# Kernel tuning notes

Hardware: AMD Instinct MI355X
Metric: run time of the kernel (lower is better)

## Reference

```python
import jax, jax.numpy as jnp
import numpy as np

NEG_INF = -jnp.inf


def setup_inputs() -> dict:
    B, T, E, H = 16, 1024, 1024, 1024  # batch, seq, embed_dim, head_dim (T <= H required by original buffer slicing)
    key = jax.random.key(0)
    k1, k2, k3, k4, k5, k6 = jax.random.split(key, 6)
    return {
        "key": jax.random.normal(k1, (B, T, E), dtype=jnp.float32),
        "query": jax.random.normal(k2, (B, T, E), dtype=jnp.float32),
        "value": jax.random.normal(k3, (B, T, E), dtype=jnp.float32),
        "padding_mask": jnp.zeros((B, 1, T), dtype=jnp.int32),
        # nn.Linear(embed_dim, head_dim, bias=False) weights: [head_dim, embed_dim]
        "Wk": jax.random.normal(k4, (H, E), dtype=jnp.float32) * (E ** -0.5),
        "Wq": jax.random.normal(k5, (H, E), dtype=jnp.float32) * (E ** -0.5),
        "Wv": jax.random.normal(k6, (H, E), dtype=jnp.float32) * (E ** -0.5),
    }


def reference(key, query, value, padding_mask, Wk, Wq, Wv):
    # key/query/value: [B, T, E]; W*: [H, E]
    B, T, E = key.shape
    k = jnp.einsum("bte,he->bth", key, Wk)
    q = jnp.einsum("bte,he->bth", query, Wq)
    v = jnp.einsum("bte,he->bth", value, Wv)
    # NOTE: original scales by d_k = key.size(-1) = embed_dim, not head_dim
    scale = 1.0 / jnp.sqrt(jnp.float32(E))
    qk = jnp.einsum("bth,bsh->bts", q, k) * scale  # [B, T, T]
    # causal buffer is tril(ones, diagonal=1): position i can attend to j <= i+1
    causal = jnp.tril(jnp.ones((T, T), dtype=jnp.float32), k=1)
    qk = jnp.where(causal == 0, NEG_INF, qk)
    qk = jnp.where(padding_mask == 1, NEG_INF, qk)  # padding_mask broadcasts [B,1,T] -> [B,T,T]
    p = jax.nn.softmax(qk, axis=-1)
    attn = jnp.einsum("bts,bsh->bth", p, v)  # dropout is identity in eval mode
    return attn
```

## Files before the change

### kernel.cpp

```cpp
#include <hip/hip_runtime.h>
#include <hip/hip_bf16.h>
#include <stdint.h>

typedef __bf16 bf16;
typedef __attribute__((ext_vector_type(8))) __bf16 bf16x8;
typedef __attribute__((ext_vector_type(4))) __bf16 bf16x4;
typedef __attribute__((ext_vector_type(4))) float  f32x4;

static __device__ __forceinline__ void gll16(const void* g, void* lds_base) {
  __builtin_amdgcn_global_load_lds((__attribute__((address_space(1))) void*)g,
                                   (__attribute__((address_space(3))) void*)lds_base,
                                   16, 0, 0);
}

#define MFMA_CLUSTER(MQ)                                                       \
  __builtin_amdgcn_s_barrier();                                                \
  asm volatile("s_waitcnt lgkmcnt(0)" ::: "memory");                           \
  __builtin_amdgcn_sched_barrier(0);                                           \
  __builtin_amdgcn_s_setprio(1);                                               \
  _Pragma("unroll") for (int i_ = 0; i_ < 4; ++i_)                             \
  _Pragma("unroll") for (int n_ = 0; n_ < 4; ++n_)                             \
  _Pragma("unroll") for (int kh_ = 0; kh_ < 2; ++kh_)                          \
    acc[(MQ) * 4 + i_][n_] = __builtin_amdgcn_mfma_f32_16x16x32_bf16(          \
        af[i_][kh_], bfr[n_][kh_], acc[(MQ) * 4 + i_][n_], 0, 0, 0);           \
  __builtin_amdgcn_s_setprio(0);

template <int VARIANT>
__global__ __launch_bounds__(512, 2) void gemm8(const bf16* __restrict__ A,
                                                const bf16* __restrict__ B,
                                                bf16* __restrict__ Cb,
                                                float* __restrict__ Cf,
                                                const int* __restrict__ pad) {
  extern __shared__ char smem[];
  char* ldsA = smem;
  char* ldsB = smem + 65536;

  const int tid = threadIdx.x;
  const int lane = tid & 63, wave = tid >> 6;
  const int lo = lane & 15, hi = lane >> 4;
  const int wmi = wave >> 2, wni = wave & 3;
  const int swz = (lo & 7) << 4;

  const int nwg = gridDim.x;
  const int id = (blockIdx.x % 8) * (nwg >> 3) + blockIdx.x / 8;

  int row0, col0, nt, b = 0;
  if (VARIANT <= 1) {
    row0 = (id >> 2) * 256; col0 = (id & 3) * 256; nt = 16;
  } else {
    b = id >> 4;
    const int r = id & 15, it = r >> 2, jt = r & 3;
    row0 = it * 256; col0 = jt * 256;
    nt = (VARIANT == 3) ? min(16, 4 * it + 6) : 16;
    if (VARIANT == 2 && jt > it + 1) return;
    if (VARIANT == 2 && jt == it + 1) {
      bf16* Sb = Cb + ((size_t)b << 20);
      bf16x8 z = {};
#pragma unroll
      for (int q = 0; q < 16; ++q) {
        const int off = (q * 512 + tid) * 8;
        *(bf16x8*)(Sb + (size_t)(row0 + (off >> 8)) * 1024 + col0 + (off & 255)) = z;
      }
      return;
    }
  }
  const bf16* Ap = A + ((size_t)b << 20) + (size_t)row0 * 1024;
  const bf16* Bp = B + ((size_t)b << 20) + (size_t)col0 * 1024;
  const int ntm1 = nt - 1;

  auto stgA = [&](int tidx, int slot) {
    const int tc = tidx > ntm1 ? ntm1 : tidx;
#pragma unroll
    for (int r = 0; r < 4; ++r) {
      const int x  = (wave * 4 + r) * 1024 + lane * 16;
      const int xs = x ^ (((x >> 7) & 7) << 4);
      gll16((const char*)Ap + (size_t)(xs >> 7) * 2048 + (size_t)tc * 128 + (xs & 127),
            ldsA + slot * 32768 + (wave * 4 + r) * 1024);
    }
  };
  auto stgB = [&](int tidx, int slot) {
    const int tc = tidx > ntm1 ? ntm1 : tidx;
#pragma unroll
    for (int r = 0; r < 4; ++r) {
      const int x  = (wave * 4 + r) * 1024 + lane * 16;
      const int xs = x ^ (((x >> 7) & 7) << 4);
      gll16((const char*)Bp + (size_t)(xs >> 7) * 2048 + (size_t)tc * 128 + (xs & 127),
            ldsB + slot * 32768 + (wave * 4 + r) * 1024);
    }
  };

  f32x4 acc[8][4] = {};

  stgB(0, 0);
  stgA(0, 0);
  stgB(1, 1);
  asm volatile("s_waitcnt vmcnt(4)" ::: "memory");
  __builtin_amdgcn_s_barrier();

  bf16x8 af[4][2], bfr[4][2];
#pragma unroll 2
  for (int u = 0; u < nt; ++u) {
    const int cur = u & 1;
#pragma unroll
    for (int i_ = 0; i_ < 4; ++i_)
#pragma unroll
      for (int kh_ = 0; kh_ < 2; ++kh_) {
        const int row_ = wmi * 128 + i_ * 16 + lo;
        af[i_][kh_] = *(const bf16x8*)(ldsA + cur * 32768 +
                                       ((row_ * 128 + kh_ * 64 + hi * 16) ^ swz));
      }
#pragma unroll
    for (int n_ = 0; n_ < 4; ++n_)
#pragma unroll
      for (int kh_ = 0; kh_ < 2; ++kh_) {
        const int row_ = wni * 64 + n_ * 16 + lo;
        bfr[n_][kh_] = *(const bf16x8*)(ldsB + cur * 32768 +
                                        ((row_ * 128 + kh_ * 64 + hi * 16) ^ swz));
      }
    stgA(u + 1, cur ^ 1);
    MFMA_CLUSTER(0)
    __builtin_amdgcn_s_barrier();
#pragma unroll
    for (int i_ = 0; i_ < 4; ++i_)
#pragma unroll
      for (int kh_ = 0; kh_ < 2; ++kh_) {
        const int row_ = wmi * 128 + 64 + i_ * 16 + lo;
        af[i_][kh_] = *(const bf16x8*)(ldsA + cur * 32768 +
                                       ((row_ * 128 + kh_ * 64 + hi * 16) ^ swz));
      }
    stgB(u + 2, cur);
    MFMA_CLUSTER(1)
    asm volatile("s_waitcnt vmcnt(4)" ::: "memory");
    __builtin_amdgcn_s_barrier();
  }

  if (VARIANT == 0) {
#pragma unroll
    for (int m = 0; m < 8; ++m)
#pragma unroll
      for (int n = 0; n < 4; ++n) {
        const int c = col0 + wni * 64 + n * 16 + lo;
        const int rbase = row0 + wmi * 128 + m * 16 + hi * 4;
#pragma unroll
        for (int j = 0; j < 4; ++j)
          Cb[(size_t)(rbase + j) * 1024 + c] = (bf16)acc[m][n][j];
      }
  } else if (VARIANT == 1) {
#pragma unroll
    for (int m = 0; m < 8; ++m)
#pragma unroll
      for (int n = 0; n < 4; ++n) {
        const int r = row0 + wmi * 128 + m * 16 + hi * 4;
        const int c = col0 + wni * 64 + n * 16 + lo;
        const int bb = r >> 10, tt = r & 1023;
        bf16x4 h = { (bf16)acc[m][n][0], (bf16)acc[m][n][1],
                     (bf16)acc[m][n][2], (bf16)acc[m][n][3] };
        *(bf16x4*)(Cb + ((size_t)bb << 20) + ((size_t)c << 10) + tt) = h;
      }
  } else if (VARIANT == 2) {
    const float NINF = -__builtin_inff();
#pragma unroll
    for (int n = 0; n < 4; ++n) {
      const int s = col0 + wni * 64 + n * 16 + lo;
      const int pd = pad[(b << 10) + s];
#pragma unroll
      for (int m = 0; m < 8; ++m) {
        const int tbase = row0 + wmi * 128 + m * 16 + hi * 4;
#pragma unroll
        for (int j = 0; j < 4; ++j) {
          float v = acc[m][n][j] * 0.03125f;
          if (s > tbase + j + 1) v = 0.f;
          else if (pd != 0) v = NINF;
          Cb[((size_t)b << 20) + (size_t)(tbase + j) * 1024 + s] = (bf16)v;
        }
      }
    }
  } else {
#pragma unroll
    for (int m = 0; m < 8; ++m)
#pragma unroll
      for (int n = 0; n < 4; ++n) {
        const int h2 = col0 + wni * 64 + n * 16 + lo;
        const int tbase = row0 + wmi * 128 + m * 16 + hi * 4;
#pragma unroll
        for (int j = 0; j < 4; ++j)
          Cf[((size_t)b << 20) + (size_t)(tbase + j) * 1024 + h2] = acc[m][n][j];
      }
  }
  asm volatile("s_waitcnt vmcnt(0)" ::: "memory");
}

__global__ __launch_bounds__(256) void cvt_kernel(const float* __restrict__ src,
                                                  bf16* __restrict__ dst, int n) {
  const int i = (blockIdx.x * 256 + threadIdx.x) * 8;
  if (i >= n) return;
  const f32x4 a = *(const f32x4*)(src + i);
  const f32x4 b = *(const f32x4*)(src + i + 4);
  bf16x8 o = { (bf16)a[0], (bf16)a[1], (bf16)a[2], (bf16)a[3],
               (bf16)b[0], (bf16)b[1], (bf16)b[2], (bf16)b[3] };
  *(bf16x8*)(dst + i) = o;
}

__global__ __launch_bounds__(256) void cvtW_kernel(const float* __restrict__ s0,
                                                   const float* __restrict__ s1,
                                                   const float* __restrict__ s2,
                                                   bf16* __restrict__ d0,
                                                   bf16* __restrict__ d1,
                                                   bf16* __restrict__ d2) {
  const int seg = blockIdx.x >> 9, blk = blockIdx.x & 511;
  const float* src = seg == 0 ? s0 : (seg == 1 ? s1 : s2);
  bf16* dst = seg == 0 ? d0 : (seg == 1 ? d1 : d2);
  const int i = (blk * 256 + threadIdx.x) * 8;
  const f32x4 a = *(const f32x4*)(src + i);
  const f32x4 b = *(const f32x4*)(src + i + 4);
  bf16x8 o = { (bf16)a[0], (bf16)a[1], (bf16)a[2], (bf16)a[3],
               (bf16)b[0], (bf16)b[1], (bf16)b[2], (bf16)b[3] };
  *(bf16x8*)(dst + i) = o;
}

__global__ __launch_bounds__(64) void corner_kernel(const bf16* __restrict__ Q,
                                                    const bf16* __restrict__ K,
                                                    const int* __restrict__ pad,
                                                    bf16* __restrict__ S) {
  const int b = blockIdx.x / 3, it = blockIdx.x % 3;
  const int t = it * 256 + 255, s = (it + 1) * 256;
  const int lane = threadIdx.x;
  const bf16* q = Q + ((size_t)b << 20) + (size_t)t * 1024 + lane * 16;
  const bf16* k = K + ((size_t)b << 20) + (size_t)s * 1024 + lane * 16;
  bf16x8 q0 = *(const bf16x8*)q, q1 = *(const bf16x8*)(q + 8);
  bf16x8 k0 = *(const bf16x8*)k, k1 = *(const bf16x8*)(k + 8);
  float d = 0.f;
#pragma unroll
  for (int j = 0; j < 8; ++j) d += (float)q0[j] * (float)k0[j] + (float)q1[j] * (float)k1[j];
#pragma unroll
  for (int o = 32; o; o >>= 1) d += __shfl_xor(d, o, 64);
  if (lane == 0) {
    float v = d * 0.03125f;
    if (pad[(b << 10) + s] != 0) v = -__builtin_inff();
    S[((size_t)b << 20) + (size_t)t * 1024 + s] = (bf16)v;
  }
}

__global__ __launch_bounds__(256) void softmax_kernel(bf16* __restrict__ S) {
  const int row  = blockIdx.x * 4 + (threadIdx.x >> 6);
  const int lane = threadIdx.x & 63;
  const int t = row & 1023;
  const int w = min(1024, t + 2);
  const bool act = lane * 16 < w;
  bf16* r = S + (size_t)row * 1024 + lane * 16;
  bf16x8 v0 = {}, v1 = {};
  float f[16];
#pragma unroll
  for (int j = 0; j < 16; ++j) f[j] = -1e30f;
  if (act) {
    v0 = *(const bf16x8*)r;
    v1 = *(const bf16x8*)(r + 8);
#pragma unroll
    for (int j = 0; j < 16; ++j)
      if (lane * 16 + j < w) f[j] = (float)(j < 8 ? v0[j] : v1[j - 8]);
  }
  float m = f[0];
#pragma unroll
  for (int j = 1; j < 16; ++j) m = fmaxf(m, f[j]);
#pragma unroll
  for (int o = 32; o; o >>= 1) m = fmaxf(m, __shfl_xor(m, o, 64));
  float sum = 0.f;
  float e[16];
#pragma unroll
  for (int j = 0; j < 16; ++j) { e[j] = __expf(f[j] - m); sum += e[j]; }
#pragma unroll
  for (int o = 32; o; o >>= 1) sum += __shfl_xor(sum, o, 64);
  const float inv = 1.0f / sum;
  if (act) {
#pragma unroll
    for (int j = 0; j < 8; ++j) {
      v0[j] = (bf16)(lane * 16 + j < w ? e[j] * inv : 0.f);
      v1[j] = (bf16)(lane * 16 + 8 + j < w ? e[8 + j] * inv : 0.f);
    }
    *(bf16x8*)r = v0;
    *(bf16x8*)(r + 8) = v1;
  }
}

extern "C" void kernel_launch(void* const* d_in, const int* in_sizes, int n_in,
                              void* d_out, int out_size, void* d_ws, size_t ws_size,
                              hipStream_t stream) {
  const float* key   = (const float*)d_in[0];
  const float* query = (const float*)d_in[1];
  const float* value = (const float*)d_in[2];
  const int*   pad   = (const int*)d_in[3];
  const float* Wk    = (const float*)d_in[4];
  const float* Wq    = (const float*)d_in[5];
  const float* Wv    = (const float*)d_in[6];
  float* out = (float*)d_out;

  bf16* Wkb = (bf16*)d_ws;
  bf16* Wqb = Wkb + (1 << 20);
  bf16* Wvb = Wqb + (1 << 20);
  bf16* qb  = Wvb + (1 << 20);
  bf16* kb  = qb  + (16 << 20);
  bf16* vT  = kb  + (16 << 20);
  bf16* S   = vT  + (16 << 20);
  bf16* Xb  = S;

  hipFuncSetAttribute(reinterpret_cast<const void*>(&gemm8<0>),
                      hipFuncAttributeMaxDynamicSharedMemorySize, 131072);
  hipFuncSetAttribute(reinterpret_cast<const void*>(&gemm8<1>),
                      hipFuncAttributeMaxDynamicSharedMemorySize, 131072);
  hipFuncSetAttribute(reinterpret_cast<const void*>(&gemm8<2>),
                      hipFuncAttributeMaxDynamicSharedMemorySize, 131072);
  hipFuncSetAttribute(reinterpret_cast<const void*>(&gemm8<3>),
                      hipFuncAttributeMaxDynamicSharedMemorySize, 131072);

  cvtW_kernel<<<1536, 256, 0, stream>>>(Wk, Wq, Wv, Wkb, Wqb, Wvb);

  cvt_kernel<<<8192, 256, 0, stream>>>(query, Xb, 16 << 20);
  gemm8<0><<<256, 512, 131072, stream>>>(Xb, Wqb, qb, nullptr, nullptr);
  cvt_kernel<<<8192, 256, 0, stream>>>(key, Xb, 16 << 20);
  gemm8<0><<<256, 512, 131072, stream>>>(Xb, Wkb, kb, nullptr, nullptr);
  cvt_kernel<<<8192, 256, 0, stream>>>(value, Xb, 16 << 20);
  gemm8<1><<<256, 512, 131072, stream>>>(Xb, Wvb, vT, nullptr, nullptr);

  gemm8<2><<<256, 512, 131072, stream>>>(qb, kb, S, nullptr, pad);
  corner_kernel<<<48, 64, 0, stream>>>(qb, kb, pad, S);
  softmax_kernel<<<4096, 256, 0, stream>>>(S);
  gemm8<3><<<256, 512, 131072, stream>>>(S, vT, nullptr, out, nullptr);
}
```

Baseline: 248.5 us.

## Fuse fp32-to-bf16 input conversion into projection GEMM A-operand staging

Removes the three standalone conversion kernels for query, key and value. The projection GEMM variants now load fp32 activations into registers, convert them to bf16 and write them into swizzled LDS, with a reworked software pipeline that splits A staging into two halves interleaved with MFMA clusters. This is meant to remove the write and re-read of the bf16 intermediate and the extra kernel launches. In exchange, the A operand loses asynchronous global-to-LDS loads, register pressure rises, and there are extra full vmcnt waits that may expose latency.

```diff
diff --git a/kernel.cpp b/kernel.cpp
--- a/kernel.cpp
+++ b/kernel.cpp
@@ -12,6 +12,11 @@
                                    (__attribute__((address_space(3))) void*)lds_base,
                                    16, 0, 0);
 }
+
+#define BARR  __builtin_amdgcn_s_barrier()
+#define VMW(N) asm volatile("s_waitcnt vmcnt(" #N ")" ::: "memory")
+#define LGKM0 asm volatile("s_waitcnt lgkmcnt(0)" ::: "memory")
+#define SB0   __builtin_amdgcn_sched_barrier(0)
 
 #define MFMA_CLUSTER(MQ)                                                       \
   __builtin_amdgcn_s_barrier();                                                \
@@ -22,15 +27,16 @@
   _Pragma("unroll") for (int n_ = 0; n_ < 4; ++n_)                             \
   _Pragma("unroll") for (int kh_ = 0; kh_ < 2; ++kh_)                          \
     acc[(MQ) * 4 + i_][n_] = __builtin_amdgcn_mfma_f32_16x16x32_bf16(          \
-        af[i_][kh_], bfr[n_][kh_], acc[(MQ) * 4 + i_][n_], 0, 0, 0);           \
+        af2[i_][kh_], bfr[n_][kh_], acc[(MQ) * 4 + i_][n_], 0, 0, 0);          \
   __builtin_amdgcn_s_setprio(0);
 
 template <int VARIANT>
-__global__ __launch_bounds__(512, 2) void gemm8(const bf16* __restrict__ A,
+__global__ __launch_bounds__(512, 2) void gemm8(const void* __restrict__ Araw,
                                                 const bf16* __restrict__ B,
                                                 bf16* __restrict__ Cb,
                                                 float* __restrict__ Cf,
                                                 const int* __restrict__ pad) {
+  constexpr bool FP32A = (VARIANT <= 1);
   extern __shared__ char smem[];
   char* ldsA = smem;
   char* ldsB = smem + 65536;
@@ -64,20 +70,12 @@
       return;
     }
   }
-  const bf16* Ap = A + ((size_t)b << 20) + (size_t)row0 * 1024;
-  const bf16* Bp = B + ((size_t)b << 20) + (size_t)col0 * 1024;
   const int ntm1 = nt - 1;
-
-  auto stgA = [&](int tidx, int slot) {
-    const int tc = tidx > ntm1 ? ntm1 : tidx;
-#pragma unroll
-    for (int r = 0; r < 4; ++r) {
-      const int x  = (wave * 4 + r) * 1024 + lane * 16;
-      const int xs = x ^ (((x >> 7) & 7) << 4);
-      gll16((const char*)Ap + (size_t)(xs >> 7) * 2048 + (size_t)tc * 128 + (xs & 127),
-            ldsA + slot * 32768 + (wave * 4 + r) * 1024);
-    }
-  };
+  const float* Afp = FP32A ? (const float*)Araw + (size_t)row0 * 1024 : nullptr;
+  const bf16*  Ab  = FP32A ? nullptr
+                           : (const bf16*)Araw + ((size_t)b << 20) + (size_t)row0 * 1024;
+  const bf16*  Bp  = B + (FP32A ? (size_t)0 : ((size_t)b << 20)) + (size_t)col0 * 1024;
+
   auto stgB = [&](int tidx, int slot) {
     const int tc = tidx > ntm1 ? ntm1 : tidx;
 #pragma unroll
@@ -88,50 +86,143 @@
             ldsB + slot * 32768 + (wave * 4 + r) * 1024);
     }
   };
+  auto stgA = [&](int tidx, int slot) {
+    const int tc = tidx > ntm1 ? ntm1 : tidx;
+#pragma unroll
+    for (int r = 0; r < 4; ++r) {
+      const int x  = (wave * 4 + r) * 1024 + lane * 16;
+      const int xs = x ^ (((x >> 7) & 7) << 4);
+      gll16((const char*)Ab + (size_t)(xs >> 7) * 2048 + (size_t)tc * 128 + (xs & 127),
+            ldsA + slot * 32768 + (wave * 4 + r) * 1024);
+    }
+  };
 
   f32x4 acc[8][4] = {};
-
-  stgB(0, 0);
-  stgA(0, 0);
-  stgB(1, 1);
-  asm volatile("s_waitcnt vmcnt(4)" ::: "memory");
-  __builtin_amdgcn_s_barrier();
-
-  bf16x8 af[4][2], bfr[4][2];
+  bf16x8 bfr[4][2];
+
+  auto rdBall = [&](int slot) {
+#pragma unroll
+    for (int n = 0; n < 4; ++n)
+#pragma unroll
+      for (int kh = 0; kh < 2; ++kh) {
+        const int row = wni * 64 + n * 16 + lo;
+        bfr[n][kh] = *(const bf16x8*)(ldsB + slot * 32768 +
+                                      ((row * 128 + kh * 64 + hi * 16) ^ swz));
+      }
+  };
+
+  if constexpr (FP32A) {
+    bf16x8 af[4];
+    f32x4 rQ[4];
+    auto glbAh = [&](int h, int t) {
+      const int tc = t > ntm1 ? ntm1 : t;
+      const float* p = Afp + (size_t)(h * 128 + (tid >> 2)) * 1024 +
+                       (size_t)tc * 64 + (tid & 3) * 16;
+      rQ[0] = *(const f32x4*)(p);
+      rQ[1] = *(const f32x4*)(p + 4);
+      rQ[2] = *(const f32x4*)(p + 8);
+      rQ[3] = *(const f32x4*)(p + 12);
+    };
+    auto wrAh = [&](int h, int slot) {
+      const int row = h * 128 + (tid >> 2);
+      const int base = row * 128 + (tid & 3) * 32;
+      const int key = (row & 7) << 4;
+      char* d = ldsA + slot * 32768;
+      bf16x8 o0 = { (bf16)rQ[0][0], (bf16)rQ[0][1], (bf16)rQ[0][2], (bf16)rQ[0][3],
+                    (bf16)rQ[1][0], (bf16)rQ[1][1], (bf16)rQ[1][2], (bf16)rQ[1][3] };
+      bf16x8 o1 = { (bf16)rQ[2][0], (bf16)rQ[2][1], (bf16)rQ[2][2], (bf16)rQ[2][3],
+                    (bf16)rQ[3][0], (bf16)rQ[3][1], (bf16)rQ[3][2], (bf16)rQ[3][3] };
+      *(bf16x8*)(d + (base ^ key)) = o0;
+      *(bf16x8*)(d + ((base + 16) ^ key)) = o1;
+    };
+    auto rdAk = [&](int mh, int kh, int slot) {
+#pragma unroll
+      for (int i = 0; i < 4; ++i) {
+        const int row = wmi * 128 + mh * 64 + i * 16 + lo;
+        af[i] = *(const bf16x8*)(ldsA + slot * 32768 +
+                                 ((row * 128 + kh * 64 + hi * 16) ^ swz));
+      }
+    };
+    auto mmaK = [&](int mh, int kh) {
+#pragma unroll
+      for (int i = 0; i < 4; ++i)
+#pragma unroll
+        for (int n = 0; n < 4; ++n)
+          acc[mh * 4 + i][n] = __builtin_amdgcn_mfma_f32_16x16x32_bf16(
+              af[i], bfr[n][kh], acc[mh * 4 + i][n], 0, 0, 0);
+    };
+
+    glbAh(0, 0); VMW(0); wrAh(0, 0);
+    glbAh(1, 0); VMW(0); wrAh(1, 0);
+    stgB(0, 0); stgB(1, 1);
+    VMW(4);
+    LGKM0; BARR;
+
 #pragma unroll 2
-  for (int u = 0; u < nt; ++u) {
-    const int cur = u & 1;
-#pragma unroll
-    for (int i_ = 0; i_ < 4; ++i_)
-#pragma unroll
-      for (int kh_ = 0; kh_ < 2; ++kh_) {
-        const int row_ = wmi * 128 + i_ * 16 + lo;
-        af[i_][kh_] = *(const bf16x8*)(ldsA + cur * 32768 +
-                                       ((row_ * 128 + kh_ * 64 + hi * 16) ^ swz));
-      }
-#pragma unroll
-    for (int n_ = 0; n_ < 4; ++n_)
-#pragma unroll
-      for (int kh_ = 0; kh_ < 2; ++kh_) {
-        const int row_ = wni * 64 + n_ * 16 + lo;
-        bfr[n_][kh_] = *(const bf16x8*)(ldsB + cur * 32768 +
-                                        ((row_ * 128 + kh_ * 64 + hi * 16) ^ swz));
-      }
-    stgA(u + 1, cur ^ 1);
-    MFMA_CLUSTER(0)
-    __builtin_amdgcn_s_barrier();
-#pragma unroll
-    for (int i_ = 0; i_ < 4; ++i_)
-#pragma unroll
-      for (int kh_ = 0; kh_ < 2; ++kh_) {
-        const int row_ = wmi * 128 + 64 + i_ * 16 + lo;
-        af[i_][kh_] = *(const bf16x8*)(ldsA + cur * 32768 +
-                                       ((row_ * 128 + kh_ * 64 + hi * 16) ^ swz));
-      }
-    stgB(u + 2, cur);
-    MFMA_CLUSTER(1)
-    asm volatile("s_waitcnt vmcnt(4)" ::: "memory");
-    __builtin_amdgcn_s_barrier();
+    for (int u = 0; u < nt; ++u) {
+      const int cur = u & 1;
+      rdAk(0, 0, cur);
+      rdBall(cur);
+      glbAh(0, u + 1);
+      BARR; LGKM0; SB0;
+      __builtin_amdgcn_s_setprio(1);
+      mmaK(0, 0);
+      rdAk(0, 1, cur); LGKM0; SB0;
+      mmaK(0, 1);
+      __builtin_amdgcn_s_setprio(0);
+      BARR;
+      rdAk(1, 0, cur);
+      VMW(0);
+      wrAh(0, cur ^ 1);
+      glbAh(1, u + 1);
+      stgB(u + 2, cur);
+      BARR; LGKM0; SB0;
+      __builtin_amdgcn_s_setprio(1);
+      mmaK(1, 0);
+      rdAk(1, 1, cur); LGKM0; SB0;
+      mmaK(1, 1);
+      __builtin_amdgcn_s_setprio(0);
+      VMW(4);
+      wrAh(1, cur ^ 1);
+      LGKM0;
+      BARR;
+    }
+  } else {
+    bf16x8 af2[4][2];
+    stgB(0, 0);
+    stgA(0, 0);
+    stgB(1, 1);
+    VMW(4);
+    BARR;
+
+#pragma unroll 2
+    for (int u = 0; u < nt; ++u) {
+      const int cur = u & 1;
+#pragma unroll
+      for (int i_ = 0; i_ < 4; ++i_)
+#pragma unroll
+        for (int kh_ = 0; kh_ < 2; ++kh_) {
+          const int row_ = wmi * 128 + i_ * 16 + lo;
+          af2[i_][kh_] = *(const bf16x8*)(ldsA + cur * 32768 +
+                                          ((row_ * 128 + kh_ * 64 + hi * 16) ^ swz));
+        }
+      rdBall(cur);
+      stgA(u + 1, cur ^ 1);
+      MFMA_CLUSTER(0)
+      BARR;
+#pragma unroll
+      for (int i_ = 0; i_ < 4; ++i_)
+#pragma unroll
+        for (int kh_ = 0; kh_ < 2; ++kh_) {
+          const int row_ = wmi * 128 + 64 + i_ * 16 + lo;
+          af2[i_][kh_] = *(const bf16x8*)(ldsA + cur * 32768 +
+                                          ((row_ * 128 + kh_ * 64 + hi * 16) ^ swz));
+        }
+      stgB(u + 2, cur);
+      MFMA_CLUSTER(1)
+      VMW(4);
+      BARR;
+    }
   }
 
   if (VARIANT == 0) {
@@ -188,17 +279,6 @@
       }
   }
   asm volatile("s_waitcnt vmcnt(0)" ::: "memory");
-}
-
-__global__ __launch_bounds__(256) void cvt_kernel(const float* __restrict__ src,
-                                                  bf16* __restrict__ dst, int n) {
-  const int i = (blockIdx.x * 256 + threadIdx.x) * 8;
-  if (i >= n) return;
-  const f32x4 a = *(const f32x4*)(src + i);
-  const f32x4 b = *(const f32x4*)(src + i + 4);
-  bf16x8 o = { (bf16)a[0], (bf16)a[1], (bf16)a[2], (bf16)a[3],
-               (bf16)b[0], (bf16)b[1], (bf16)b[2], (bf16)b[3] };
-  *(bf16x8*)(dst + i) = o;
 }
 
 __global__ __launch_bounds__(256) void cvtW_kernel(const float* __restrict__ s0,
@@ -301,7 +381,6 @@
   bf16* kb  = qb  + (16 << 20);
   bf16* vT  = kb  + (16 << 20);
   bf16* S   = vT  + (16 << 20);
-  bf16* Xb  = S;
 
   hipFuncSetAttribute(reinterpret_cast<const void*>(&gemm8<0>),
                       hipFuncAttributeMaxDynamicSharedMemorySize, 131072);
@@ -314,15 +393,12 @@
 
   cvtW_kernel<<<1536, 256, 0, stream>>>(Wk, Wq, Wv, Wkb, Wqb, Wvb);
 
-  cvt_kernel<<<8192, 256, 0, stream>>>(query, Xb, 16 << 20);
-  gemm8<0><<<256, 512, 131072, stream>>>(Xb, Wqb, qb, nullptr, nullptr);
-  cvt_kernel<<<8192, 256, 0, stream>>>(key, Xb, 16 << 20);
-  gemm8<0><<<256, 512, 131072, stream>>>(Xb, Wkb, kb, nullptr, nullptr);
-  cvt_kernel<<<8192, 256, 0, stream>>>(value, Xb, 16 << 20);
-  gemm8<1><<<256, 512, 131072, stream>>>(Xb, Wvb, vT, nullptr, nullptr);
-
-  gemm8<2><<<256, 512, 131072, stream>>>(qb, kb, S, nullptr, pad);
+  gemm8<0><<<256, 512, 131072, stream>>>((const void*)query, Wqb, qb, nullptr, nullptr);
+  gemm8<0><<<256, 512, 131072, stream>>>((const void*)key,   Wkb, kb, nullptr, nullptr);
+  gemm8<1><<<256, 512, 131072, stream>>>((const void*)value, Wvb, vT, nullptr, nullptr);
+
+  gemm8<2><<<256, 512, 131072, stream>>>((const void*)qb, kb, S, nullptr, pad);
   corner_kernel<<<48, 64, 0, stream>>>(qb, kb, pad, S);
   softmax_kernel<<<4096, 256, 0, stream>>>(S);
-  gemm8<3><<<256, 512, 131072, stream>>>(S, vT, nullptr, out, nullptr);
-}
+  gemm8<3><<<256, 512, 131072, stream>>>((const void*)S, vT, nullptr, out, nullptr);
+}
```

Measured after the change: 338.0 us. 1.36x slower.

## Batch QKV projections into one launch and halve GEMM K-tile to 32

Applied to the files above, without the earlier changes.

The three input conversions are merged into a single launch, and the three projection GEMMs are merged into one 768-workgroup launch that picks operands per segment, with V written transposed. The output buffer is borrowed as scratch for the converted key and value. The GEMM K-tile is cut from 64 to 32, so LDS drops to 64 KB and the loop runs twice as many iterations with a narrower swizzle. The aim is fewer launches, more resident workgroups and better fill across CUs, at the cost of more barriers per unit of work.

```diff
diff --git a/kernel.cpp b/kernel.cpp
--- a/kernel.cpp
+++ b/kernel.cpp
@@ -13,48 +13,56 @@
                                    16, 0, 0);
 }
 
-#define MFMA_CLUSTER(MQ)                                                       \
-  __builtin_amdgcn_s_barrier();                                                \
-  asm volatile("s_waitcnt lgkmcnt(0)" ::: "memory");                           \
-  __builtin_amdgcn_sched_barrier(0);                                           \
-  __builtin_amdgcn_s_setprio(1);                                               \
-  _Pragma("unroll") for (int i_ = 0; i_ < 4; ++i_)                             \
-  _Pragma("unroll") for (int n_ = 0; n_ < 4; ++n_)                             \
-  _Pragma("unroll") for (int kh_ = 0; kh_ < 2; ++kh_)                          \
-    acc[(MQ) * 4 + i_][n_] = __builtin_amdgcn_mfma_f32_16x16x32_bf16(          \
-        af[i_][kh_], bfr[n_][kh_], acc[(MQ) * 4 + i_][n_], 0, 0, 0);           \
-  __builtin_amdgcn_s_setprio(0);
+#define BARR  __builtin_amdgcn_s_barrier()
+#define VMW(N) asm volatile("s_waitcnt vmcnt(" #N ")" ::: "memory")
+#define LGKM0 asm volatile("s_waitcnt lgkmcnt(0)" ::: "memory")
+#define SB0   __builtin_amdgcn_sched_barrier(0)
 
 template <int VARIANT>
-__global__ __launch_bounds__(512, 2) void gemm8(const bf16* __restrict__ A,
-                                                const bf16* __restrict__ B,
-                                                bf16* __restrict__ Cb,
+__global__ __launch_bounds__(512, 2) void gemm8(const bf16* __restrict__ a0,
+                                                const bf16* __restrict__ a1,
+                                                const bf16* __restrict__ a2,
+                                                const bf16* __restrict__ b0,
+                                                const bf16* __restrict__ b1,
+                                                const bf16* __restrict__ b2,
+                                                bf16* __restrict__ c0,
+                                                bf16* __restrict__ c1,
+                                                bf16* __restrict__ c2,
                                                 float* __restrict__ Cf,
                                                 const int* __restrict__ pad) {
   extern __shared__ char smem[];
   char* ldsA = smem;
-  char* ldsB = smem + 65536;
+  char* ldsB = smem + 32768;
 
   const int tid = threadIdx.x;
   const int lane = tid & 63, wave = tid >> 6;
   const int lo = lane & 15, hi = lane >> 4;
   const int wmi = wave >> 2, wni = wave & 3;
-  const int swz = (lo & 7) << 4;
+  const int swz = (lo & 3) << 4;
 
   const int nwg = gridDim.x;
   const int id = (blockIdx.x % 8) * (nwg >> 3) + blockIdx.x / 8;
 
-  int row0, col0, nt, b = 0;
-  if (VARIANT <= 1) {
-    row0 = (id >> 2) * 256; col0 = (id & 3) * 256; nt = 16;
+  int row0, col0, nt, batch = 0, trans = 0;
+  const bf16 *Ap, *Bp;
+  bf16* Cb;
+  if (VARIANT == 0) {
+    const int seg = id >> 8, idl = id & 255;
+    row0 = (idl >> 2) * 256; col0 = (idl & 3) * 256; nt = 32;
+    trans = (seg == 2);
+    const bf16* As = seg == 0 ? a0 : (seg == 1 ? a1 : a2);
+    const bf16* Bs = seg == 0 ? b0 : (seg == 1 ? b1 : b2);
+    Cb = seg == 0 ? c0 : (seg == 1 ? c1 : c2);
+    Ap = As + (size_t)row0 * 1024;
+    Bp = Bs + (size_t)col0 * 1024;
   } else {
-    b = id >> 4;
+    batch = id >> 4;
     const int r = id & 15, it = r >> 2, jt = r & 3;
     row0 = it * 256; col0 = jt * 256;
-    nt = (VARIANT == 3) ? min(16, 4 * it + 6) : 16;
+    nt = (VARIANT == 3) ? min(32, 8 * it + 10) : 32;
     if (VARIANT == 2 && jt > it + 1) return;
     if (VARIANT == 2 && jt == it + 1) {
-      bf16* Sb = Cb + ((size_t)b << 20);
+      bf16* Sb = c0 + ((size_t)batch << 20);
       bf16x8 z = {};
 #pragma unroll
       for (int q = 0; q < 16; ++q) {
@@ -63,106 +71,105 @@
       }
       return;
     }
-  }
-  const bf16* Ap = A + ((size_t)b << 20) + (size_t)row0 * 1024;
-  const bf16* Bp = B + ((size_t)b << 20) + (size_t)col0 * 1024;
+    Ap = a0 + ((size_t)batch << 20) + (size_t)row0 * 1024;
+    Bp = b0 + ((size_t)batch << 20) + (size_t)col0 * 1024;
+    Cb = c0;
+  }
   const int ntm1 = nt - 1;
 
-  auto stgA = [&](int tidx, int slot) {
+  auto stg = [&](const bf16* base, char* ldsOp, int tidx, int slot) {
     const int tc = tidx > ntm1 ? ntm1 : tidx;
 #pragma unroll
-    for (int r = 0; r < 4; ++r) {
-      const int x  = (wave * 4 + r) * 1024 + lane * 16;
-      const int xs = x ^ (((x >> 7) & 7) << 4);
-      gll16((const char*)Ap + (size_t)(xs >> 7) * 2048 + (size_t)tc * 128 + (xs & 127),
-            ldsA + slot * 32768 + (wave * 4 + r) * 1024);
+    for (int r = 0; r < 2; ++r) {
+      const int x  = wave * 2048 + r * 1024 + lane * 16;
+      const int xs = x ^ (((x >> 6) & 3) << 4);
+      gll16((const char*)base + (size_t)(xs >> 6) * 2048 + (size_t)tc * 64 + (xs & 63),
+            ldsOp + slot * 16384 + wave * 2048 + r * 1024);
     }
   };
-  auto stgB = [&](int tidx, int slot) {
-    const int tc = tidx > ntm1 ? ntm1 : tidx;
-#pragma unroll
-    for (int r = 0; r < 4; ++r) {
-      const int x  = (wave * 4 + r) * 1024 + lane * 16;
-      const int xs = x ^ (((x >> 7) & 7) << 4);
-      gll16((const char*)Bp + (size_t)(xs >> 7) * 2048 + (size_t)tc * 128 + (xs & 127),
-            ldsB + slot * 32768 + (wave * 4 + r) * 1024);
+
+  f32x4 acc[8][4] = {};
+  bf16x8 af[4], bfr[4];
+
+  auto rdA = [&](int mh, int slot) {
+#pragma unroll
+    for (int i = 0; i < 4; ++i) {
+      const int row = wmi * 128 + mh * 64 + i * 16 + lo;
+      af[i] = *(const bf16x8*)(ldsA + slot * 16384 + ((row * 64 + hi * 16) ^ swz));
     }
   };
-
-  f32x4 acc[8][4] = {};
-
-  stgB(0, 0);
-  stgA(0, 0);
-  stgB(1, 1);
-  asm volatile("s_waitcnt vmcnt(4)" ::: "memory");
-  __builtin_amdgcn_s_barrier();
-
-  bf16x8 af[4][2], bfr[4][2];
+  auto rdB = [&](int slot) {
+#pragma unroll
+    for (int n = 0; n < 4; ++n) {
+      const int row = wni * 64 + n * 16 + lo;
+      bfr[n] = *(const bf16x8*)(ldsB + slot * 16384 + ((row * 64 + hi * 16) ^ swz));
+    }
+  };
+  auto mmaQ = [&](int mh) {
+    __builtin_amdgcn_s_setprio(1);
+#pragma unroll
+    for (int i = 0; i < 4; ++i)
+#pragma unroll
+      for (int n = 0; n < 4; ++n)
+        acc[mh * 4 + i][n] = __builtin_amdgcn_mfma_f32_16x16x32_bf16(
+            af[i], bfr[n], acc[mh * 4 + i][n], 0, 0, 0);
+    __builtin_amdgcn_s_setprio(0);
+  };
+
+  stg(Bp, ldsB, 0, 0);
+  stg(Ap, ldsA, 0, 0);
+  stg(Bp, ldsB, 1, 1);
+  VMW(2);
+  BARR;
+
 #pragma unroll 2
   for (int u = 0; u < nt; ++u) {
     const int cur = u & 1;
-#pragma unroll
-    for (int i_ = 0; i_ < 4; ++i_)
-#pragma unroll
-      for (int kh_ = 0; kh_ < 2; ++kh_) {
-        const int row_ = wmi * 128 + i_ * 16 + lo;
-        af[i_][kh_] = *(const bf16x8*)(ldsA + cur * 32768 +
-                                       ((row_ * 128 + kh_ * 64 + hi * 16) ^ swz));
-      }
-#pragma unroll
-    for (int n_ = 0; n_ < 4; ++n_)
-#pragma unroll
-      for (int kh_ = 0; kh_ < 2; ++kh_) {
-        const int row_ = wni * 64 + n_ * 16 + lo;
-        bfr[n_][kh_] = *(const bf16x8*)(ldsB + cur * 32768 +
-                                        ((row_ * 128 + kh_ * 64 + hi * 16) ^ swz));
-      }
-    stgA(u + 1, cur ^ 1);
-    MFMA_CLUSTER(0)
-    __builtin_amdgcn_s_barrier();
-#pragma unroll
-    for (int i_ = 0; i_ < 4; ++i_)
-#pragma unroll
-      for (int kh_ = 0; kh_ < 2; ++kh_) {
-        const int row_ = wmi * 128 + 64 + i_ * 16 + lo;
-        af[i_][kh_] = *(const bf16x8*)(ldsA + cur * 32768 +
-                                       ((row_ * 128 + kh_ * 64 + hi * 16) ^ swz));
-      }
-    stgB(u + 2, cur);
-    MFMA_CLUSTER(1)
-    asm volatile("s_waitcnt vmcnt(4)" ::: "memory");
-    __builtin_amdgcn_s_barrier();
+    rdA(0, cur);
+    rdB(cur);
+    stg(Ap, ldsA, u + 1, cur ^ 1);
+    BARR; LGKM0; SB0;
+    mmaQ(0);
+    BARR;
+    rdA(1, cur);
+    stg(Bp, ldsB, u + 2, cur);
+    BARR; LGKM0; SB0;
+    mmaQ(1);
+    VMW(2);
+    BARR;
   }
 
   if (VARIANT == 0) {
-#pragma unroll
-    for (int m = 0; m < 8; ++m)
-#pragma unroll
-      for (int n = 0; n < 4; ++n) {
-        const int c = col0 + wni * 64 + n * 16 + lo;
-        const int rbase = row0 + wmi * 128 + m * 16 + hi * 4;
-#pragma unroll
-        for (int j = 0; j < 4; ++j)
-          Cb[(size_t)(rbase + j) * 1024 + c] = (bf16)acc[m][n][j];
-      }
-  } else if (VARIANT == 1) {
-#pragma unroll
-    for (int m = 0; m < 8; ++m)
-#pragma unroll
-      for (int n = 0; n < 4; ++n) {
-        const int r = row0 + wmi * 128 + m * 16 + hi * 4;
-        const int c = col0 + wni * 64 + n * 16 + lo;
-        const int bb = r >> 10, tt = r & 1023;
-        bf16x4 h = { (bf16)acc[m][n][0], (bf16)acc[m][n][1],
-                     (bf16)acc[m][n][2], (bf16)acc[m][n][3] };
-        *(bf16x4*)(Cb + ((size_t)bb << 20) + ((size_t)c << 10) + tt) = h;
-      }
+    if (!trans) {
+#pragma unroll
+      for (int m = 0; m < 8; ++m)
+#pragma unroll
+        for (int n = 0; n < 4; ++n) {
+          const int c = col0 + wni * 64 + n * 16 + lo;
+          const int rbase = row0 + wmi * 128 + m * 16 + hi * 4;
+#pragma unroll
+          for (int j = 0; j < 4; ++j)
+            Cb[(size_t)(rbase + j) * 1024 + c] = (bf16)acc[m][n][j];
+        }
+    } else {
+#pragma unroll
+      for (int m = 0; m < 8; ++m)
+#pragma unroll
+        for (int n = 0; n < 4; ++n) {
+          const int r = row0 + wmi * 128 + m * 16 + hi * 4;
+          const int c = col0 + wni * 64 + n * 16 + lo;
+          const int bb = r >> 10, tt = r & 1023;
+          bf16x4 h = { (bf16)acc[m][n][0], (bf16)acc[m][n][1],
+                       (bf16)acc[m][n][2], (bf16)acc[m][n][3] };
+          *(bf16x4*)(Cb + ((size_t)bb << 20) + ((size_t)c << 10) + tt) = h;
+        }
+    }
   } else if (VARIANT == 2) {
     const float NINF = -__builtin_inff();
 #pragma unroll
     for (int n = 0; n < 4; ++n) {
       const int s = col0 + wni * 64 + n * 16 + lo;
-      const int pd = pad[(b << 10) + s];
+      const int pd = pad[(batch << 10) + s];
 #pragma unroll
       for (int m = 0; m < 8; ++m) {
         const int tbase = row0 + wmi * 128 + m * 16 + hi * 4;
@@ -171,7 +178,7 @@
           float v = acc[m][n][j] * 0.03125f;
           if (s > tbase + j + 1) v = 0.f;
           else if (pd != 0) v = NINF;
-          Cb[((size_t)b << 20) + (size_t)(tbase + j) * 1024 + s] = (bf16)v;
+          Cb[((size_t)batch << 20) + (size_t)(tbase + j) * 1024 + s] = (bf16)v;
         }
       }
     }
@@ -184,16 +191,22 @@
         const int tbase = row0 + wmi * 128 + m * 16 + hi * 4;
 #pragma unroll
         for (int j = 0; j < 4; ++j)
-          Cf[((size_t)b << 20) + (size_t)(tbase + j) * 1024 + h2] = acc[m][n][j];
+          Cf[((size_t)batch << 20) + (size_t)(tbase + j) * 1024 + h2] = acc[m][n][j];
       }
   }
   asm volatile("s_waitcnt vmcnt(0)" ::: "memory");
 }
 
-__global__ __launch_bounds__(256) void cvt_kernel(const float* __restrict__ src,
-                                                  bf16* __restrict__ dst, int n) {
-  const int i = (blockIdx.x * 256 + threadIdx.x) * 8;
-  if (i >= n) return;
+__global__ __launch_bounds__(256) void cvt3_kernel(const float* __restrict__ s0,
+                                                   const float* __restrict__ s1,
+                                                   const float* __restrict__ s2,
+                                                   bf16* __restrict__ d0,
+                                                   bf16* __restrict__ d1,
+                                                   bf16* __restrict__ d2) {
+  const int seg = blockIdx.x >> 13, blk = blockIdx.x & 8191;
+  const float* src = seg == 0 ? s0 : (seg == 1 ? s1 : s2);
+  bf16* dst = seg == 0 ? d0 : (seg == 1 ? d1 : d2);
+  const int i = (blk * 256 + threadIdx.x) * 8;
   const f32x4 a = *(const f32x4*)(src + i);
   const f32x4 b = *(const f32x4*)(src + i + 4);
   bf16x8 o = { (bf16)a[0], (bf16)a[1], (bf16)a[2], (bf16)a[3],
@@ -301,28 +314,27 @@
   bf16* kb  = qb  + (16 << 20);
   bf16* vT  = kb  + (16 << 20);
   bf16* S   = vT  + (16 << 20);
-  bf16* Xb  = S;
+  bf16* Xq  = S;
+  bf16* Xk  = (bf16*)d_out;
+  bf16* Xv  = Xk + (16 << 20);
 
   hipFuncSetAttribute(reinterpret_cast<const void*>(&gemm8<0>),
-                      hipFuncAttributeMaxDynamicSharedMemorySize, 131072);
-  hipFuncSetAttribute(reinterpret_cast<const void*>(&gemm8<1>),
-                      hipFuncAttributeMaxDynamicSharedMemorySize, 131072);
+                      hipFuncAttributeMaxDynamicSharedMemorySize, 65536);
   hipFuncSetAttribute(reinterpret_cast<const void*>(&gemm8<2>),
-                      hipFuncAttributeMaxDynamicSharedMemorySize, 131072);
+                      hipFuncAttributeMaxDynamicSharedMemorySize, 65536);
   hipFuncSetAttribute(reinterpret_cast<const void*>(&gemm8<3>),
-                      hipFuncAttributeMaxDynamicSharedMemorySize, 131072);
+                      hipFuncAttributeMaxDynamicSharedMemorySize, 65536);
 
   cvtW_kernel<<<1536, 256, 0, stream>>>(Wk, Wq, Wv, Wkb, Wqb, Wvb);
-
-  cvt_kernel<<<8192, 256, 0, stream>>>(query, Xb, 16 << 20);
-  gemm8<0><<<256, 512, 131072, stream>>>(Xb, Wqb, qb, nullptr, nullptr);
-  cvt_kernel<<<8192, 256, 0, stream>>>(key, Xb, 16 << 20);
-  gemm8<0><<<256, 512, 131072, stream>>>(Xb, Wkb, kb, nullptr, nullptr);
-  cvt_kernel<<<8192, 256, 0, stream>>>(value, Xb, 16 << 20);
-  gemm8<1><<<256, 512, 131072, stream>>>(Xb, Wvb, vT, nullptr, nullptr);
-
-  gemm8<2><<<256, 512, 131072, stream>>>(qb, kb, S, nullptr, pad);
+  cvt3_kernel<<<24576, 256, 0, stream>>>(query, key, value, Xq, Xk, Xv);
+
+  gemm8<0><<<768, 512, 65536, stream>>>(Xq, Xk, Xv, Wqb, Wkb, Wvb,
+                                        qb, kb, vT, nullptr, nullptr);
+
+  gemm8<2><<<256, 512, 65536, stream>>>(qb, nullptr, nullptr, kb, nullptr, nullptr,
+                                        S, nullptr, nullptr, nullptr, pad);
   corner_kernel<<<48, 64, 0, stream>>>(qb, kb, pad, S);
   softmax_kernel<<<4096, 256, 0, stream>>>(S);
-  gemm8<3><<<256, 512, 131072, stream>>>(S, vT, nullptr, out, nullptr);
-}
+  gemm8<3><<<256, 512, 65536, stream>>>(S, nullptr, nullptr, vT, nullptr, nullptr,
+                                        nullptr, nullptr, nullptr, out, nullptr);
+}
```

Result: no change. 249.9 us (+0.5%).
